# Performance work log

Hardware: AMD Instinct MI355X
Metric: run time of the kernel (lower is better)

Reference implementation:

```python
import jax, jax.numpy as jnp
import numpy as np
from jax import lax

I = 834      # inputSize
H = 190      # rnnHiddenstateSize
F = 250      # fastNnHiddensize
O = 512      # outputSize
T = 256      # number of sequential steps


def setup_inputs() -> dict:
    key = jax.random.key(0)
    ks = jax.random.split(key, 10)
    x = jax.random.normal(ks[0], (T, I), jnp.float32)
    h0 = jax.random.normal(ks[1], (H,), jnp.float32) * 0.0005          # rnnInitialHiddenstate
    Wrnn = jax.random.normal(ks[2], (H, H + I), jnp.float32) * 0.002   # rnnWeightMatrix
    brnn = jax.random.normal(ks[3], (H,), jnp.float32) * 0.02          # rnnBiasVector
    Wupd = jax.random.normal(ks[4], ((I + H) * F, H), jnp.float32) * 0.05  # ffnnWeightupdateCalcWeightMatrix
    bupd = jax.random.normal(ks[5], ((I + H) * F,), jnp.float32) * 0.05    # ffnnWeightupdateCalcBias
    # FastNn params (fc1 kaiming-uniform approx: U(-b, b), b = sqrt(6/fan_in))
    bound = float(np.sqrt(6.0 / (I + H)))
    W1 = jax.random.uniform(ks[6], (I + H, F), jnp.float32, -bound, bound)
    b1 = jnp.zeros((F,), jnp.float32)
    W2 = jax.random.normal(ks[7], (F, O), jnp.float32) * 0.02
    b2 = jnp.zeros((O,), jnp.float32)
    return {"x": x, "h0": h0, "Wrnn": Wrnn, "brnn": brnn,
            "Wupd": Wupd, "bupd": bupd, "W1": W1, "b1": b1, "W2": W2, "b2": b2}


def reference(x, h0, Wrnn, brnn, Wupd, bupd, W1, b1, W2, b2):
    # Sequential fast-weight RNN: per step the FastNn fc1 weight is updated by a
    # delta computed from the RNN hidden state. Output of step t uses the
    # fast-weight BEFORE the step-t update (matches original ordering).
    def step(carry, xt):
        h, fw1 = carry
        # RNN cell: concat(h, x) order as in original
        h_new = jnp.tanh(jnp.concatenate([h, xt]) @ Wrnn.T + brnn)       # [H]
        # weight-update GEMV (dominant memory traffic: [(I+H)*F, H] matrix)
        delta = (Wupd @ h_new + bupd).reshape(fw1.shape)                  # [I+H, F]
        # FastNn forward: concat(x, h_new) order as in original
        fast_in = jnp.concatenate([xt, h_new])                            # [I+H]
        out = jax.nn.selu(fast_in @ fw1 + b1) @ W2 + b2                   # [O]
        return (h_new, fw1 + delta), out

    (_, _), outs = lax.scan(step, (h0, W1), x)
    return outs  # [T, O]
```

## Files before the change

kernel.cpp:

```cpp
#include <hip/hip_runtime.h>
#include <hip/hip_bf16.h>

#define I_SZ 834
#define H_SZ 190
#define F_SZ 250
#define O_SZ 512
#define T_SZ 256
#define K_SZ 1024
#define NW   47500


typedef __attribute__((ext_vector_type(8))) short short8;
typedef __attribute__((ext_vector_type(4))) float f32x4;

__device__ __forceinline__ short f2bf(float f) {
    union { __hip_bfloat16 h; short s; } u;
    u.h = __float2bfloat16(f);
    return u.s;
}
__device__ __forceinline__ float bf2f(short s) {
    union { short s; __hip_bfloat16 h; } u;
    u.s = s;
    return __bfloat162float(u.h);
}

__device__ __forceinline__ void gll16(const void* g, void* l) {
    __builtin_amdgcn_global_load_lds(
        (const __attribute__((address_space(1))) void*)g,
        (__attribute__((address_space(3))) void*)l, 16, 0, 0);
}

__device__ __forceinline__ void lds_barrier() {
    asm volatile("s_waitcnt lgkmcnt(0)" ::: "memory");
    __builtin_amdgcn_s_barrier();
}

__device__ __forceinline__ float fast_tanh(float x) {
    const float e = __expf(2.f * x);
    return 1.f - 2.f / (e + 1.f);
}

__global__ void __launch_bounds__(256) k2b_buildAx(const float* __restrict__ x,
                                                   const float* __restrict__ W1,
                                                   const float* __restrict__ bupd,
                                                   const float* __restrict__ W2,
                                                   const float* __restrict__ Wrnn,
                                                   short* __restrict__ Abf2,
                                                   float* __restrict__ zprime,
                                                   float* __restrict__ W1p,
                                                   float* __restrict__ bupdp,
                                                   short* __restrict__ W2s,
                                                   short* __restrict__ Wxs) {
    const int t = blockIdx.x;
    const int c = threadIdx.x;
    for (int i = c; i < I_SZ; i += 256)
        Abf2[(i >> 3) * (T_SZ * 8) + t * 8 + (i & 7)] = f2bf(x[t * I_SZ + i]);
    for (int i = I_SZ + c; i < 864; i += 256)
        Abf2[(i >> 3) * (T_SZ * 8) + t * 8 + (i & 7)] = 0;
    for (int j = c; j < F_SZ; j += 256)
        zprime[t * F_SZ + j] = 0.f;
    #pragma unroll
    for (int rr = 0; rr < 4; ++rr) {
        const int r = t * 4 + rr;
        W1p[r * 256 + c]   = (c < F_SZ) ? W1[r * F_SZ + c] : 0.f;
        bupdp[r * 256 + c] = (c < F_SZ) ? bupd[r * F_SZ + c] : 0.f;
    }
    {
        const int j = t;
        #pragma unroll
        for (int rep = 0; rep < 2; ++rep) {
            const int o = c + rep * 256;
            W2s[(j >> 3) * (O_SZ * 8) + o * 8 + (j & 7)] =
                (j < F_SZ) ? f2bf(W2[j * O_SZ + o]) : (short)0;
        }
    }
    if (t < 108) {
        const int h = c;
        if (h < 192) {
            #pragma unroll
            for (int e = 0; e < 8; ++e) {
                const int kk = t * 8 + e;
                const float v = (h < H_SZ && kk < I_SZ) ? Wrnn[h * K_SZ + H_SZ + kk] : 0.f;
                Wxs[t * 1536 + h * 8 + e] = f2bf(v);
            }
        }
    }
}

__global__ void __launch_bounds__(256) k1_mfma(const short* __restrict__ Abf2,
                                               const short* __restrict__ Wxs,
                                               const float* __restrict__ brnn,
                                               float* __restrict__ P) {
    const int tid = threadIdx.x;
    const int bh = blockIdx.x;
    const int w = tid >> 6, l = tid & 63;
    const int l15 = l & 15, lg = l >> 4;

    f32x4 acc[4];
    #pragma unroll
    for (int tt = 0; tt < 4; ++tt) acc[tt] = (f32x4){0.f, 0.f, 0.f, 0.f};

    for (int ks = 0; ks < 27; ++ks) {
        const short8 afr = *reinterpret_cast<const short8*>(
            &Wxs[(size_t)(ks * 4 + lg) * 1536 + (size_t)(bh * 16 + l15) * 8]);
        #pragma unroll
        for (int tt = 0; tt < 4; ++tt) {
            const short* ap = Abf2 + (size_t)(ks * 4 + lg) * (T_SZ * 8)
                                   + (size_t)(w * 64 + tt * 16 + l15) * 8;
            short8 bfr = *reinterpret_cast<const short8*>(ap);
            acc[tt] = __builtin_amdgcn_mfma_f32_16x16x32_bf16(afr, bfr, acc[tt], 0, 0, 0);
        }
    }
    #pragma unroll
    for (int tt = 0; tt < 4; ++tt) {
        const int t = w * 64 + tt * 16 + l15;
        #pragma unroll
        for (int r = 0; r < 4; ++r) {
            const int hrow = bh * 16 + lg * 4 + r;
            if (hrow < H_SZ) P[t * H_SZ + hrow] = acc[tt][r] + brnn[hrow];
        }
    }
}

__global__ void __launch_bounds__(768, 1) k2_scan(const float* __restrict__ Wrnn,
                                                  const float* __restrict__ h0,
                                                  const float* __restrict__ P,
                                                  float* __restrict__ S,
                                                  short* __restrict__ Abf2) {
    __shared__ __align__(16) short hlds[2][192];
    const int tid = threadIdx.x;
    const int w = tid >> 6, l = tid & 63;
    const int l15 = l & 15, lg = l >> 4;
    const short8 zs = {0, 0, 0, 0, 0, 0, 0, 0};
    const int n = w * 16 + l15;
    const bool nok = n < H_SZ;

    short8 B[6];
    #pragma unroll
    for (int kt = 0; kt < 6; ++kt) {
        short8 bf = zs;
        #pragma unroll
        for (int e = 0; e < 8; ++e) {
            const int kk = kt * 32 + lg * 8 + e;
            float v = (nok && kk < H_SZ) ? Wrnn[n * K_SZ + kk] : 0.f;
            bf[e] = f2bf(v);
        }
        B[kt] = bf;
    }
    if (tid < 192) {
        hlds[0][tid] = f2bf((tid < H_SZ) ? h0[tid] : 0.f);
        hlds[1][tid] = 0;
    }
    float Srun = 0.f;
    float pc = (l < 16 && nok) ? P[n] : 0.f;
    lds_barrier();

    int rb = 0;
    #pragma unroll 1
    for (int t = 0; t < T_SZ; ++t) {
        short8 a[6];
        #pragma unroll
        for (int kt = 0; kt < 6; ++kt) {
            short8 ar = *reinterpret_cast<const short8*>(&hlds[rb][kt * 32 + lg * 8]);
            a[kt] = (l15 == 0) ? ar : zs;
        }
        const float pn = (t + 1 < T_SZ && l < 16 && nok) ? P[(t + 1) * H_SZ + n] : 0.f;
        f32x4 c[6];
        #pragma unroll
        for (int kt = 0; kt < 6; ++kt) {
            const f32x4 z4 = {0.f, 0.f, 0.f, 0.f};
            c[kt] = __builtin_amdgcn_mfma_f32_16x16x32_bf16(a[kt], B[kt], z4, 0, 0, 0);
        }
        if (l < 16 && nok) {
            const float s = ((c[0][0] + c[1][0]) + (c[2][0] + c[3][0]))
                          + (c[4][0] + c[5][0]) + pc;
            const float v = fast_tanh(s);
            S[t * H_SZ + n] = Srun;
            const int k = I_SZ + n;
            Abf2[(k >> 3) * (T_SZ * 8) + t * 8 + (k & 7)] = f2bf(v);
            hlds[rb ^ 1][n] = f2bf(v);
            Srun += v;
        }
        lds_barrier();
        rb ^= 1;
        pc = pn;
    }
}

__global__ void __launch_bounds__(512) k3_mfma(const float* __restrict__ Wupd,
                                               const float* __restrict__ W1p,
                                               const float* __restrict__ bupdp,
                                               const short* __restrict__ Abf2,
                                               const float* __restrict__ S,
                                               float* __restrict__ zprime,
                                               float* __restrict__ d1,
                                               float* __restrict__ d2h,
                                               float* __restrict__ d2l) {
    __shared__ __align__(16) float Wlds[2][4096];
    __shared__ __align__(16) short Alds[2][8192];
    __shared__ float part[2][256];
    const int tid = threadIdx.x;
    const int bid = blockIdx.x;
    const bool mainb = bid < 372;
    const int role = mainb ? 0 : (bid - 372);
    const int mat  = role >> 1;
    const bool isLo = (!mainb) && (mat == 2);
    const float* Wsrc = mainb ? Wupd : ((mat == 0) ? W1p : bupdp);
    const int stride  = mainb ? NW : 256;
    const int ncols   = mainb ? NW : 256;
    const int bn0     = mainb ? bid * 128 : (role & 1) * 128;
    const int l = tid & 63, wv = tid >> 6;
    const int l15 = l & 15, lg = l >> 4;

    part[tid >> 8][tid & 255] = 0.f;

    const char* src[4];
    long long stp[4];
    int cloc[4];
    #pragma unroll
    for (int i = 0; i < 4; ++i) {
        const int c = wv * 4 + i;
        cloc[i] = c;
        if (c < 16) {
            const int k = c * 2 + (l >> 5);
            const int n = (l & 31) * 4;
            const bool ok = (bn0 + n + 4) <= ncols;
            src[i] = (const char*)(Wsrc + (size_t)k * stride + (ok ? (size_t)(bn0 + n) : 0));
            stp[i] = (long long)32 * stride * 4;
        } else {
            src[i] = (const char*)(Abf2 + (size_t)(c - 16) * 512 + (size_t)l * 8);
            stp[i] = 16384;
        }
    }

    f32x4 acc[16];
    #pragma unroll
    for (int tt = 0; tt < 16; ++tt) acc[tt] = (f32x4){0.f, 0.f, 0.f, 0.f};

    #pragma unroll
    for (int i = 0; i < 4; ++i) {
        void* dst = (cloc[i] < 16) ? (void*)&Wlds[0][cloc[i] * 256]
                                   : (void*)&Alds[0][(cloc[i] - 16) * 512];
        gll16(src[i], dst);
        src[i] += stp[i];
    }
    __syncthreads();

    int cur = 0;
    #pragma unroll 1
    for (int s = 0; s < 32; ++s) {
        if (s + 1 < 32) {
            #pragma unroll
            for (int i = 0; i < 4; ++i) {
                void* dst = (cloc[i] < 16) ? (void*)&Wlds[cur ^ 1][cloc[i] * 256]
                                           : (void*)&Alds[cur ^ 1][(cloc[i] - 16) * 512];
                gll16(src[i], dst);
                src[i] += stp[i];
            }
        }
        short8 afr;
        if (isLo) {
            #pragma unroll
            for (int e = 0; e < 8; ++e) {
                const float v = Wlds[cur][(lg * 8 + e) * 128 + wv * 16 + l15];
                afr[e] = f2bf(v - bf2f(f2bf(v)));
            }
        } else {
            #pragma unroll
            for (int e = 0; e < 8; ++e)
                afr[e] = f2bf(Wlds[cur][(lg * 8 + e) * 128 + wv * 16 + l15]);
        }
        #pragma unroll
        for (int tt = 0; tt < 16; ++tt) {
            short8 bfr = *reinterpret_cast<const short8*>(
                &Alds[cur][((size_t)lg * 256 + tt * 16 + l15) * 8]);
            acc[tt] = __builtin_amdgcn_mfma_f32_16x16x32_bf16(afr, bfr, acc[tt], 0, 0, 0);
        }
        __syncthreads();
        cur ^= 1;
    }

    if (mainb) {
        const int jlo = bn0 / H_SZ;
        #pragma unroll
        for (int tt = 0; tt < 16; ++tt) {
            float p0 = 0.f, p1 = 0.f;
            const int t = tt * 16 + l15;
            #pragma unroll
            for (int r = 0; r < 4; ++r) {
                const int n = bn0 + wv * 16 + lg * 4 + r;
                const bool ok = n < NW;
                const int nc = ok ? n : NW - 1;
                const int j = nc / H_SZ;
                const int h = nc - j * H_SZ;
                const float sv = S[t * H_SZ + h];
                const float prod = ok ? acc[tt][r] * sv : 0.f;
                if (j == jlo) p0 += prod; else p1 += prod;
            }
            p0 += __shfl_xor(p0, 16, 64); p0 += __shfl_xor(p0, 32, 64);
            p1 += __shfl_xor(p1, 16, 64); p1 += __shfl_xor(p1, 32, 64);
            if (lg == 0) {
                if (p0 != 0.f) atomicAdd(&part[0][t], p0);
                if (p1 != 0.f) atomicAdd(&part[1][t], p1);
            }
        }
        __syncthreads();
        const int b = tid >> 8, t = tid & 255;
        const int j = jlo + b;
        const float v = part[b][t];
        if (j < F_SZ && v != 0.f) atomicAdd(&zprime[t * F_SZ + j], v);
    } else {
        float* dst = (mat == 0) ? d1 : ((mat == 1) ? d2h : d2l);
        #pragma unroll
        for (int tt = 0; tt < 16; ++tt) {
            const int t = tt * 16 + l15;
            #pragma unroll
            for (int r = 0; r < 4; ++r) {
                const int n = bn0 + wv * 16 + lg * 4 + r;
                if (n < F_SZ) dst[t * 256 + n] = acc[tt][r];
            }
        }
    }
}

__global__ void __launch_bounds__(256) k4e_selu(const float* __restrict__ zprime,
                                                const float* __restrict__ d1,
                                                const float* __restrict__ d2h,
                                                const float* __restrict__ d2l,
                                                const float* __restrict__ b1,
                                                short* __restrict__ ysb) {
    const int t = blockIdx.x;
    const int j = threadIdx.x;
    short sv = 0;
    if (j < F_SZ) {
        const float d2 = d2h[t * 256 + j] + d2l[t * 256 + j];
        float z = zprime[t * F_SZ + j] + d1[t * 256 + j] + (float)t * d2 + b1[j];
        const float scale = 1.0507009873554805f, alpha = 1.6732632423543772f;
        float y = z > 0.f ? scale * z : scale * alpha * (expf(z) - 1.f);
        sv = f2bf(y);
    }
    ysb[(j >> 3) * (T_SZ * 8) + t * 8 + (j & 7)] = sv;
}

__global__ void __launch_bounds__(64) k4b_mfma(const short* __restrict__ ysb,
                                               const short* __restrict__ W2s,
                                               const float* __restrict__ b2,
                                               float* __restrict__ out) {
    const int l = threadIdx.x;
    const int o0 = (blockIdx.x & 31) * 16;
    const int th = blockIdx.x >> 5;
    const int l15 = l & 15, lg = l >> 4;
    const int o = o0 + l15;

    f32x4 acc[2];
    acc[0] = (f32x4){0.f, 0.f, 0.f, 0.f};
    acc[1] = (f32x4){0.f, 0.f, 0.f, 0.f};

    #pragma unroll
    for (int ks = 0; ks < 8; ++ks) {
        const short8 afr = *reinterpret_cast<const short8*>(
            &W2s[(size_t)(ks * 4 + lg) * (O_SZ * 8) + (size_t)o * 8]);
        #pragma unroll
        for (int tt = 0; tt < 2; ++tt) {
            const short* ap = ysb + (size_t)(ks * 4 + lg) * (T_SZ * 8)
                                  + (size_t)(th * 32 + tt * 16 + l15) * 8;
            short8 bfr = *reinterpret_cast<const short8*>(ap);
            acc[tt] = __builtin_amdgcn_mfma_f32_16x16x32_bf16(afr, bfr, acc[tt], 0, 0, 0);
        }
    }
    #pragma unroll
    for (int tt = 0; tt < 2; ++tt) {
        const int t = th * 32 + tt * 16 + l15;
        #pragma unroll
        for (int r = 0; r < 4; ++r) {
            const int oo = o0 + lg * 4 + r;
            out[t * O_SZ + oo] = acc[tt][r] + b2[oo];
        }
    }
}

extern "C" void kernel_launch(void* const* d_in, const int* in_sizes, int n_in,
                              void* d_out, int out_size, void* d_ws, size_t ws_size,
                              hipStream_t stream) {
    const float* x    = (const float*)d_in[0];
    const float* h0   = (const float*)d_in[1];
    const float* Wrnn = (const float*)d_in[2];
    const float* brnn = (const float*)d_in[3];
    const float* Wupd = (const float*)d_in[4];
    const float* bupd = (const float*)d_in[5];
    const float* W1   = (const float*)d_in[6];
    const float* b1   = (const float*)d_in[7];
    const float* W2   = (const float*)d_in[8];
    const float* b2   = (const float*)d_in[9];
    float* out = (float*)d_out;

    float* ws = (float*)d_ws;
    float* P      = ws;
    float* S      = P + T_SZ * H_SZ;
    float* zprime = S + T_SZ * H_SZ;
    short* Abf2   = (short*)(zprime + T_SZ * F_SZ);
    short* ysb    = Abf2 + 262144;
    float* d1     = (float*)(ysb + 65536);
    float* d2h    = d1 + 65536;
    float* d2l    = d2h + 65536;
    float* W1p    = d2l + 65536;
    float* bupdp  = W1p + 262144;
    short* W2s    = (short*)(bupdp + 262144);
    short* Wxs    = W2s + 131072;

    k2b_buildAx<<<T_SZ, 256, 0, stream>>>(x, W1, bupd, W2, Wrnn,
                                          Abf2, zprime, W1p, bupdp, W2s, Wxs);
    k1_mfma    <<<12,   256, 0, stream>>>(Abf2, Wxs, brnn, P);
    k2_scan    <<<1,    768, 0, stream>>>(Wrnn, h0, P, S, Abf2);
    k3_mfma    <<<378,  512, 0, stream>>>(Wupd, W1p, bupdp, Abf2, S, zprime, d1, d2h, d2l);
    k4e_selu   <<<T_SZ, 256, 0, stream>>>(zprime, d1, d2h, d2l, b1, ysb);
    k4b_mfma   <<<256,  64,  0, stream>>>(ysb, W2s, b2, out);
}
```

Before: 261.7 us.

## Fuse RNN scan into weight-update GEMM kernel with flag-based overlap

Merges the single-block recurrent scan and the large Wupd GEMM into one launch. Block 0 runs the scan, now with 512 threads and a split-K over two wave groups. The other blocks stream the first 26 K-slices of Wupd, which come from the input part and do not need the hidden state, then spin on a global flag until the scan finishes before processing the last 6 slices. GEMM blocks are widened to 256 columns so the grid fits co-resident. This hides scan latency behind memory streaming, but risks deadlock if not all blocks are resident, and adds spin-wait overhead.

```diff
diff --git a/kernel.cpp b/kernel.cpp
--- a/kernel.cpp
+++ b/kernel.cpp
@@ -8,7 +8,6 @@
 #define T_SZ 256
 #define K_SZ 1024
 #define NW   47500
-
 
 typedef __attribute__((ext_vector_type(8))) short short8;
 typedef __attribute__((ext_vector_type(4))) float f32x4;
@@ -50,9 +49,11 @@
                                                    float* __restrict__ W1p,
                                                    float* __restrict__ bupdp,
                                                    short* __restrict__ W2s,
-                                                   short* __restrict__ Wxs) {
+                                                   short* __restrict__ Wxs,
+                                                   unsigned int* __restrict__ flag) {
     const int t = blockIdx.x;
     const int c = threadIdx.x;
+    if (t == 0 && c == 0) *flag = 0u;
     for (int i = c; i < I_SZ; i += 256)
         Abf2[(i >> 3) * (T_SZ * 8) + t * 8 + (i & 7)] = f2bf(x[t * I_SZ + i]);
     for (int i = I_SZ + c; i < 864; i += 256)
@@ -74,15 +75,12 @@
                 (j < F_SZ) ? f2bf(W2[j * O_SZ + o]) : (short)0;
         }
     }
-    if (t < 108) {
-        const int h = c;
-        if (h < 192) {
-            #pragma unroll
-            for (int e = 0; e < 8; ++e) {
-                const int kk = t * 8 + e;
-                const float v = (h < H_SZ && kk < I_SZ) ? Wrnn[h * K_SZ + H_SZ + kk] : 0.f;
-                Wxs[t * 1536 + h * 8 + e] = f2bf(v);
-            }
+    if (t < 108 && c < 192) {
+        #pragma unroll
+        for (int e = 0; e < 8; ++e) {
+            const int kk = t * 8 + e;
+            const float v = (c < H_SZ && kk < I_SZ) ? Wrnn[c * K_SZ + H_SZ + kk] : 0.f;
+            Wxs[t * 1536 + c * 8 + e] = f2bf(v);
         }
     }
 }
@@ -122,204 +120,245 @@
     }
 }
 
-__global__ void __launch_bounds__(768, 1) k2_scan(const float* __restrict__ Wrnn,
-                                                  const float* __restrict__ h0,
-                                                  const float* __restrict__ P,
-                                                  float* __restrict__ S,
-                                                  short* __restrict__ Abf2) {
+__global__ void __launch_bounds__(512, 2) k23_fused(
+        const float* __restrict__ Wrnn, const float* __restrict__ h0,
+        const float* __restrict__ P, float* __restrict__ S,
+        short* __restrict__ Abf2,
+        const float* __restrict__ Wupd, const float* __restrict__ W1p,
+        const float* __restrict__ bupdp,
+        float* __restrict__ zprime, float* __restrict__ d1,
+        float* __restrict__ d2h, float* __restrict__ d2l,
+        unsigned int* __restrict__ flag) {
+    __shared__ __align__(16) float Wlds[2][32 * 256];
+    __shared__ __align__(16) short Alds[2][8192];
+    __shared__ float part3[3][256];
     __shared__ __align__(16) short hlds[2][192];
-    const int tid = threadIdx.x;
-    const int w = tid >> 6, l = tid & 63;
-    const int l15 = l & 15, lg = l >> 4;
-    const short8 zs = {0, 0, 0, 0, 0, 0, 0, 0};
-    const int n = w * 16 + l15;
-    const bool nok = n < H_SZ;
-
-    short8 B[6];
-    #pragma unroll
-    for (int kt = 0; kt < 6; ++kt) {
-        short8 bf = zs;
-        #pragma unroll
-        for (int e = 0; e < 8; ++e) {
-            const int kk = kt * 32 + lg * 8 + e;
-            float v = (nok && kk < H_SZ) ? Wrnn[n * K_SZ + kk] : 0.f;
-            bf[e] = f2bf(v);
-        }
-        B[kt] = bf;
-    }
-    if (tid < 192) {
-        hlds[0][tid] = f2bf((tid < H_SZ) ? h0[tid] : 0.f);
-        hlds[1][tid] = 0;
-    }
-    float Srun = 0.f;
-    float pc = (l < 16 && nok) ? P[n] : 0.f;
-    lds_barrier();
-
-    int rb = 0;
-    #pragma unroll 1
-    for (int t = 0; t < T_SZ; ++t) {
-        short8 a[6];
-        #pragma unroll
-        for (int kt = 0; kt < 6; ++kt) {
-            short8 ar = *reinterpret_cast<const short8*>(&hlds[rb][kt * 32 + lg * 8]);
-            a[kt] = (l15 == 0) ? ar : zs;
-        }
-        const float pn = (t + 1 < T_SZ && l < 16 && nok) ? P[(t + 1) * H_SZ + n] : 0.f;
-        f32x4 c[6];
-        #pragma unroll
-        for (int kt = 0; kt < 6; ++kt) {
-            const f32x4 z4 = {0.f, 0.f, 0.f, 0.f};
-            c[kt] = __builtin_amdgcn_mfma_f32_16x16x32_bf16(a[kt], B[kt], z4, 0, 0, 0);
-        }
-        if (l < 16 && nok) {
-            const float s = ((c[0][0] + c[1][0]) + (c[2][0] + c[3][0]))
-                          + (c[4][0] + c[5][0]) + pc;
-            const float v = fast_tanh(s);
-            S[t * H_SZ + n] = Srun;
-            const int k = I_SZ + n;
-            Abf2[(k >> 3) * (T_SZ * 8) + t * 8 + (k & 7)] = f2bf(v);
-            hlds[rb ^ 1][n] = f2bf(v);
-            Srun += v;
-        }
-        lds_barrier();
-        rb ^= 1;
-        pc = pn;
-    }
-}
-
-__global__ void __launch_bounds__(512) k3_mfma(const float* __restrict__ Wupd,
-                                               const float* __restrict__ W1p,
-                                               const float* __restrict__ bupdp,
-                                               const short* __restrict__ Abf2,
-                                               const float* __restrict__ S,
-                                               float* __restrict__ zprime,
-                                               float* __restrict__ d1,
-                                               float* __restrict__ d2h,
-                                               float* __restrict__ d2l) {
-    __shared__ __align__(16) float Wlds[2][4096];
-    __shared__ __align__(16) short Alds[2][8192];
-    __shared__ float part[2][256];
+    __shared__ float spart[2][192];
+
     const int tid = threadIdx.x;
     const int bid = blockIdx.x;
-    const bool mainb = bid < 372;
-    const int role = mainb ? 0 : (bid - 372);
-    const int mat  = role >> 1;
-    const bool isLo = (!mainb) && (mat == 2);
-    const float* Wsrc = mainb ? Wupd : ((mat == 0) ? W1p : bupdp);
-    const int stride  = mainb ? NW : 256;
-    const int ncols   = mainb ? NW : 256;
-    const int bn0     = mainb ? bid * 128 : (role & 1) * 128;
-    const int l = tid & 63, wv = tid >> 6;
+    const int l = tid & 63;
     const int l15 = l & 15, lg = l >> 4;
 
-    part[tid >> 8][tid & 255] = 0.f;
-
-    const char* src[4];
-    long long stp[4];
-    int cloc[4];
-    #pragma unroll
-    for (int i = 0; i < 4; ++i) {
-        const int c = wv * 4 + i;
+    if (bid == 0) {
+        const int w = tid >> 6;
+        const int wn = w & 3, wk = w >> 2;
+        const short8 zs = {0, 0, 0, 0, 0, 0, 0, 0};
+        short8 B[3][3];
+        #pragma unroll
+        for (int kt = 0; kt < 3; ++kt)
+            #pragma unroll
+            for (int nt = 0; nt < 3; ++nt) {
+                const int n = wn * 48 + nt * 16 + l15;
+                short8 bf = zs;
+                #pragma unroll
+                for (int e = 0; e < 8; ++e) {
+                    const int kk = wk * 96 + kt * 32 + lg * 8 + e;
+                    float v = (n < H_SZ && kk < H_SZ) ? Wrnn[n * K_SZ + kk] : 0.f;
+                    bf[e] = f2bf(v);
+                }
+                B[kt][nt] = bf;
+            }
+        if (tid < 192) {
+            hlds[0][tid] = f2bf((tid < H_SZ) ? h0[tid] : 0.f);
+            hlds[1][tid] = 0;
+        }
+        float Srun = 0.f;
+        float pc = (tid < H_SZ) ? P[tid] : 0.f;
+        lds_barrier();
+
+        int rb = 0;
+        #pragma unroll 1
+        for (int t = 0; t < T_SZ; ++t) {
+            short8 a[3];
+            #pragma unroll
+            for (int kt = 0; kt < 3; ++kt) {
+                short8 ar = *reinterpret_cast<const short8*>(
+                    &hlds[rb][wk * 96 + kt * 32 + lg * 8]);
+                a[kt] = (l15 == 0) ? ar : zs;
+            }
+            const float pn = (t + 1 < T_SZ && tid < H_SZ) ? P[(t + 1) * H_SZ + tid] : 0.f;
+            f32x4 acc[3];
+            #pragma unroll
+            for (int nt = 0; nt < 3; ++nt) {
+                f32x4 c4 = {0.f, 0.f, 0.f, 0.f};
+                #pragma unroll
+                for (int kt = 0; kt < 3; ++kt)
+                    c4 = __builtin_amdgcn_mfma_f32_16x16x32_bf16(a[kt], B[kt][nt], c4, 0, 0, 0);
+                acc[nt] = c4;
+            }
+            if (l < 16) {
+                #pragma unroll
+                for (int nt = 0; nt < 3; ++nt)
+                    spart[wk][wn * 48 + nt * 16 + l] = acc[nt][0];
+            }
+            lds_barrier();
+            if (tid < H_SZ) {
+                const float v = fast_tanh(spart[0][tid] + spart[1][tid] + pc);
+                S[t * H_SZ + tid] = Srun;
+                const int k = I_SZ + tid;
+                Abf2[(k >> 3) * (T_SZ * 8) + t * 8 + (k & 7)] = f2bf(v);
+                hlds[rb ^ 1][tid] = f2bf(v);
+                Srun += v;
+            }
+            lds_barrier();
+            rb ^= 1;
+            pc = pn;
+        }
+        __threadfence();
+        if (tid == 0) atomicExch(flag, 1u);
+        return;
+    }
+
+    const bool mainb = bid <= 186;
+    const int role = mainb ? 0 : (bid - 187);
+    const bool isLo = (!mainb) && (role == 2);
+    const float* Wsrc = mainb ? Wupd : ((role == 0) ? W1p : bupdp);
+    const long long stride = mainb ? NW : 256;
+    const int ncols = mainb ? NW : 256;
+    const int bn0 = mainb ? (bid - 1) * 256 : 0;
+    const int wv = tid >> 6;
+
+    for (int i = tid; i < 768; i += 512) (&part3[0][0])[i] = 0.f;
+
+    const char* src[6];
+    long long stp[6];
+    int cloc[6];
+    #pragma unroll
+    for (int i = 0; i < 6; ++i) {
+        const int c = wv * 6 + i;
         cloc[i] = c;
-        if (c < 16) {
-            const int k = c * 2 + (l >> 5);
-            const int n = (l & 31) * 4;
-            const bool ok = (bn0 + n + 4) <= ncols;
-            src[i] = (const char*)(Wsrc + (size_t)k * stride + (ok ? (size_t)(bn0 + n) : 0));
-            stp[i] = (long long)32 * stride * 4;
+        if (c < 32) {
+            const int col = l * 4;
+            const bool ok = (bn0 + col + 4) <= ncols;
+            src[i] = (const char*)(Wsrc + (size_t)c * stride + (size_t)(ok ? (bn0 + col) : bn0));
+            stp[i] = 32LL * stride * 4;
         } else {
-            src[i] = (const char*)(Abf2 + (size_t)(c - 16) * 512 + (size_t)l * 8);
+            const int ca = c - 32;
+            src[i] = (const char*)(Abf2 + (size_t)ca * 512 + (size_t)l * 8);
             stp[i] = 16384;
         }
     }
 
-    f32x4 acc[16];
-    #pragma unroll
-    for (int tt = 0; tt < 16; ++tt) acc[tt] = (f32x4){0.f, 0.f, 0.f, 0.f};
-
-    #pragma unroll
-    for (int i = 0; i < 4; ++i) {
-        void* dst = (cloc[i] < 16) ? (void*)&Wlds[0][cloc[i] * 256]
-                                   : (void*)&Alds[0][(cloc[i] - 16) * 512];
-        gll16(src[i], dst);
-        src[i] += stp[i];
-    }
+    f32x4 acc[2][16];
+    #pragma unroll
+    for (int hf = 0; hf < 2; ++hf)
+        #pragma unroll
+        for (int tt = 0; tt < 16; ++tt) acc[hf][tt] = (f32x4){0.f, 0.f, 0.f, 0.f};
+
+#define K23_ISSUE(BUF) do {                                                    \
+        _Pragma("unroll")                                                      \
+        for (int i = 0; i < 6; ++i) {                                          \
+            void* dst = (cloc[i] < 32) ? (void*)&Wlds[BUF][cloc[i] * 256]      \
+                                       : (void*)&Alds[BUF][(cloc[i] - 32) * 512]; \
+            gll16(src[i], dst);                                                \
+            src[i] += stp[i];                                                  \
+        }                                                                      \
+    } while (0)
+
+#define K23_COMPUTE(BUF) do {                                                  \
+        short8 afr0, afr1;                                                     \
+        _Pragma("unroll")                                                      \
+        for (int e = 0; e < 8; ++e) {                                          \
+            const float v0 = Wlds[BUF][(lg * 8 + e) * 256 + wv * 16 + l15];    \
+            const float v1 = Wlds[BUF][(lg * 8 + e) * 256 + 128 + wv * 16 + l15]; \
+            if (isLo) {                                                        \
+                afr0[e] = f2bf(v0 - bf2f(f2bf(v0)));                           \
+                afr1[e] = f2bf(v1 - bf2f(f2bf(v1)));                           \
+            } else {                                                           \
+                afr0[e] = f2bf(v0);                                            \
+                afr1[e] = f2bf(v1);                                            \
+            }                                                                  \
+        }                                                                      \
+        _Pragma("unroll")                                                      \
+        for (int tt = 0; tt < 16; ++tt) {                                      \
+            short8 bfr = *reinterpret_cast<const short8*>(                     \
+                &Alds[BUF][((size_t)lg * 256 + tt * 16 + l15) * 8]);           \
+            acc[0][tt] = __builtin_amdgcn_mfma_f32_16x16x32_bf16(afr0, bfr, acc[0][tt], 0, 0, 0); \
+            acc[1][tt] = __builtin_amdgcn_mfma_f32_16x16x32_bf16(afr1, bfr, acc[1][tt], 0, 0, 0); \
+        }                                                                      \
+    } while (0)
+
+    K23_ISSUE(0);
     __syncthreads();
-
     int cur = 0;
     #pragma unroll 1
-    for (int s = 0; s < 32; ++s) {
-        if (s + 1 < 32) {
-            #pragma unroll
-            for (int i = 0; i < 4; ++i) {
-                void* dst = (cloc[i] < 16) ? (void*)&Wlds[cur ^ 1][cloc[i] * 256]
-                                           : (void*)&Alds[cur ^ 1][(cloc[i] - 16) * 512];
-                gll16(src[i], dst);
-                src[i] += stp[i];
-            }
-        }
-        short8 afr;
-        if (isLo) {
-            #pragma unroll
-            for (int e = 0; e < 8; ++e) {
-                const float v = Wlds[cur][(lg * 8 + e) * 128 + wv * 16 + l15];
-                afr[e] = f2bf(v - bf2f(f2bf(v)));
-            }
-        } else {
-            #pragma unroll
-            for (int e = 0; e < 8; ++e)
-                afr[e] = f2bf(Wlds[cur][(lg * 8 + e) * 128 + wv * 16 + l15]);
-        }
-        #pragma unroll
-        for (int tt = 0; tt < 16; ++tt) {
-            short8 bfr = *reinterpret_cast<const short8*>(
-                &Alds[cur][((size_t)lg * 256 + tt * 16 + l15) * 8]);
-            acc[tt] = __builtin_amdgcn_mfma_f32_16x16x32_bf16(afr, bfr, acc[tt], 0, 0, 0);
-        }
+    for (int s = 0; s < 26; ++s) {
+        if (s < 25) K23_ISSUE(cur ^ 1);
+        K23_COMPUTE(cur);
         __syncthreads();
         cur ^= 1;
     }
 
+    if (tid == 0) {
+        while (atomicAdd(flag, 0u) == 0u) __builtin_amdgcn_s_sleep(32);
+    }
+    __syncthreads();
+    __threadfence();
+
+    K23_ISSUE(cur);
+    __syncthreads();
+    #pragma unroll 1
+    for (int s = 26; s < 32; ++s) {
+        if (s < 31) K23_ISSUE(cur ^ 1);
+        K23_COMPUTE(cur);
+        __syncthreads();
+        cur ^= 1;
+    }
+#undef K23_ISSUE
+#undef K23_COMPUTE
+
     if (mainb) {
         const int jlo = bn0 / H_SZ;
         #pragma unroll
-        for (int tt = 0; tt < 16; ++tt) {
-            float p0 = 0.f, p1 = 0.f;
-            const int t = tt * 16 + l15;
+        for (int hf = 0; hf < 2; ++hf) {
             #pragma unroll
-            for (int r = 0; r < 4; ++r) {
-                const int n = bn0 + wv * 16 + lg * 4 + r;
-                const bool ok = n < NW;
-                const int nc = ok ? n : NW - 1;
-                const int j = nc / H_SZ;
-                const int h = nc - j * H_SZ;
-                const float sv = S[t * H_SZ + h];
-                const float prod = ok ? acc[tt][r] * sv : 0.f;
-                if (j == jlo) p0 += prod; else p1 += prod;
-            }
-            p0 += __shfl_xor(p0, 16, 64); p0 += __shfl_xor(p0, 32, 64);
-            p1 += __shfl_xor(p1, 16, 64); p1 += __shfl_xor(p1, 32, 64);
-            if (lg == 0) {
-                if (p0 != 0.f) atomicAdd(&part[0][t], p0);
-                if (p1 != 0.f) atomicAdd(&part[1][t], p1);
+            for (int tt = 0; tt < 16; ++tt) {
+                float p0 = 0.f, p1 = 0.f, p2 = 0.f;
+                const int t = tt * 16 + l15;
+                #pragma unroll
+                for (int r = 0; r < 4; ++r) {
+                    const int n = bn0 + hf * 128 + wv * 16 + lg * 4 + r;
+                    const bool ok = n < NW;
+                    const int nc = ok ? n : NW - 1;
+                    const int j = nc / H_SZ;
+                    const int h = nc - j * H_SZ;
+                    const float prod = ok ? acc[hf][tt][r] * S[t * H_SZ + h] : 0.f;
+                    const int b = j - jlo;
+                    if (b == 0) p0 += prod;
+                    else if (b == 1) p1 += prod;
+                    else p2 += prod;
+                }
+                p0 += __shfl_xor(p0, 16, 64); p0 += __shfl_xor(p0, 32, 64);
+                p1 += __shfl_xor(p1, 16, 64); p1 += __shfl_xor(p1, 32, 64);
+                p2 += __shfl_xor(p2, 16, 64); p2 += __shfl_xor(p2, 32, 64);
+                if (lg == 0) {
+                    if (p0 != 0.f) atomicAdd(&part3[0][t], p0);
+                    if (p1 != 0.f) atomicAdd(&part3[1][t], p1);
+                    if (p2 != 0.f) atomicAdd(&part3[2][t], p2);
+                }
             }
         }
         __syncthreads();
-        const int b = tid >> 8, t = tid & 255;
-        const int j = jlo + b;
-        const float v = part[b][t];
-        if (j < F_SZ && v != 0.f) atomicAdd(&zprime[t * F_SZ + j], v);
+        for (int i = tid; i < 768; i += 512) {
+            const int b = i >> 8, t = i & 255;
+            const int j = jlo + b;
+            const float v = part3[b][t];
+            if (j < F_SZ && v != 0.f) atomicAdd(&zprime[t * F_SZ + j], v);
+        }
     } else {
-        float* dst = (mat == 0) ? d1 : ((mat == 1) ? d2h : d2l);
-        #pragma unroll
-        for (int tt = 0; tt < 16; ++tt) {
-            const int t = tt * 16 + l15;
+        float* dst = (role == 0) ? d1 : ((role == 1) ? d2h : d2l);
+        #pragma unroll
+        for (int hf = 0; hf < 2; ++hf)
             #pragma unroll
-            for (int r = 0; r < 4; ++r) {
-                const int n = bn0 + wv * 16 + lg * 4 + r;
-                if (n < F_SZ) dst[t * 256 + n] = acc[tt][r];
-            }
-        }
+            for (int tt = 0; tt < 16; ++tt) {
+                const int t = tt * 16 + l15;
+                #pragma unroll
+                for (int r = 0; r < 4; ++r) {
+                    const int n = hf * 128 + wv * 16 + lg * 4 + r;
+                    dst[t * 256 + n] = acc[hf][tt][r];
+                }
+            }
     }
 }
 
@@ -407,12 +446,13 @@
     float* bupdp  = W1p + 262144;
     short* W2s    = (short*)(bupdp + 262144);
     short* Wxs    = W2s + 131072;
+    unsigned int* flag = (unsigned int*)(Wxs + 165888);
 
     k2b_buildAx<<<T_SZ, 256, 0, stream>>>(x, W1, bupd, W2, Wrnn,
-                                          Abf2, zprime, W1p, bupdp, W2s, Wxs);
+                                          Abf2, zprime, W1p, bupdp, W2s, Wxs, flag);
     k1_mfma    <<<12,   256, 0, stream>>>(Abf2, Wxs, brnn, P);
-    k2_scan    <<<1,    768, 0, stream>>>(Wrnn, h0, P, S, Abf2);
-    k3_mfma    <<<378,  512, 0, stream>>>(Wupd, W1p, bupdp, Abf2, S, zprime, d1, d2h, d2l);
+    k23_fused  <<<190,  512, 0, stream>>>(Wrnn, h0, P, S, Abf2,
+                                          Wupd, W1p, bupdp, zprime, d1, d2h, d2l, flag);
     k4e_selu   <<<T_SZ, 256, 0, stream>>>(zprime, d1, d2h, d2l, b1, ysb);
     k4b_mfma   <<<256,  64,  0, stream>>>(ysb, W2s, b2, out);
 }
```

Result: no change. 264.7 us (+1.1%).
